# Kernel tuning notes

Hardware: AMD Instinct MI355X
Metric: run time of the kernel (lower is better)

The kernel has to match this reference:

```python
import jax, jax.numpy as jnp
import numpy as np

EMBED = 1024
HEADS = 16
HEAD_DIM = EMBED // HEADS


def setup_inputs() -> dict:
    key = jax.random.key(0)
    ks = jax.random.split(key, 8)
    B, S = 2, 2048
    inp = {
        "values": jax.random.normal(ks[0], (B, S, EMBED), jnp.float32),
        "keys": jax.random.normal(ks[1], (B, S, EMBED), jnp.float32),
        "queries": jax.random.normal(ks[2], (B, S, EMBED), jnp.float32),
        # per-head projection weights (torch Linear: y = x @ W.T), shared across heads
        "Wv": jax.random.normal(ks[3], (HEAD_DIM, HEAD_DIM), jnp.float32) / np.sqrt(HEAD_DIM),
        "Wk": jax.random.normal(ks[4], (HEAD_DIM, HEAD_DIM), jnp.float32) / np.sqrt(HEAD_DIM),
        "Wq": jax.random.normal(ks[5], (HEAD_DIM, HEAD_DIM), jnp.float32) / np.sqrt(HEAD_DIM),
        "Wo": jax.random.normal(ks[6], (EMBED, EMBED), jnp.float32) / np.sqrt(EMBED),
        "bo": jax.random.normal(ks[7], (EMBED,), jnp.float32) * 0.02,
    }
    return inp


def reference(values, keys, queries, Wv, Wk, Wq, Wo, bo):
    B, S, _ = queries.shape
    # split heads: (B, H, S, D)
    def split(x):
        return x.reshape(B, -1, HEADS, HEAD_DIM).transpose(0, 2, 1, 3)
    v, k, q = split(values), split(keys), split(queries)
    # per-head linear projections (no bias): x @ W.T
    v = jnp.einsum('bhsd,ed->bhse', v, Wv)
    k = jnp.einsum('bhsd,ed->bhse', k, Wk)
    q = jnp.einsum('bhsd,ed->bhse', q, Wq)
    # scaled dot-product attention (naive, full matrix)
    scores = jnp.einsum('bhqd,bhkd->bhqk', q, k) / jnp.sqrt(jnp.float32(HEAD_DIM))
    attn = jax.nn.softmax(scores, axis=-1)
    out = jnp.einsum('bhqk,bhkd->bhqd', attn, v)
    # merge heads and output projection
    out = out.transpose(0, 2, 1, 3).reshape(B, S, EMBED)
    return out @ Wo.T + bo
```

## Files before the change

kernel.cpp:

```cpp
#include <hip/hip_runtime.h>
#include <stdint.h>

#define HEADS 16
#define HD    64
#define SEQ   2048
#define BATCH 2
#define EMB   1024

using short8  = __attribute__((ext_vector_type(8))) short;
using float4v = __attribute__((ext_vector_type(4))) float;
using f32x16  = __attribute__((ext_vector_type(16))) float;

__device__ __forceinline__ unsigned int f2bfr(float f) {
    return (__float_as_uint(f) + 0x8000u) >> 16;
}

__device__ __forceinline__ unsigned int cvt_pk_bf16(float lo, float hi) {
    unsigned int r;
    asm("v_cvt_pk_bf16_f32 %0, %1, %2" : "=v"(r) : "v"(lo), "v"(hi));
    return r;
}

__device__ __forceinline__ short8 mk8(unsigned int a, unsigned int b,
                                      unsigned int c, unsigned int d) {
    union { unsigned int u[4]; short8 s; } x;
    x.u[0] = a; x.u[1] = b; x.u[2] = c; x.u[3] = d;
    return x.s;
}

__global__ __launch_bounds__(256) void cvt_wo_kernel(const float* __restrict__ Wo,
                                                     unsigned short* __restrict__ Wob) {
    int i = (blockIdx.x * 256 + threadIdx.x) * 4;
    float4 v = *(const float4*)(Wo + i);
    uint2 o;
    o.x = f2bfr(v.x) | (f2bfr(v.y) << 16);
    o.y = f2bfr(v.z) | (f2bfr(v.w) << 16);
    *(uint2*)(Wob + i) = o;
}

__global__ __launch_bounds__(256) void proj_kernel(
    const float* __restrict__ Vx, const float* __restrict__ Kx, const float* __restrict__ Qx,
    const float* __restrict__ Wv, const float* __restrict__ Wk, const float* __restrict__ Wq,
    unsigned short* __restrict__ Qp, unsigned short* __restrict__ Kp,
    unsigned short* __restrict__ Vt) {
    __shared__ __align__(16) unsigned short Ws[64 * 72];
    __shared__ __align__(16) unsigned short xs[64 * 72];
    __shared__ __align__(16) unsigned short vt2[64 * 72];

    const int t = threadIdx.x, w = t >> 6, lane = t & 63, cl = lane & 15, quad = lane >> 4;
    const int z  = blockIdx.z;
    const int bh = blockIdx.y;
    const int b  = bh >> 4, h = bh & 15;
    const int s0 = blockIdx.x * 64;

    const float* x = (z == 0) ? Qx : (z == 1) ? Kx : Vx;
    const float* W = (z == 0) ? Wq : (z == 1) ? Wk : Wv;
    const float scale = (z == 0) ? 0.18033688011112044f : 1.0f;

#pragma unroll
    for (int rep = 0; rep < 4; ++rep) {
        int idx = rep * 1024 + t * 4;
        int e = idx >> 6, d0 = idx & 63;
        float4 w4 = *(const float4*)(W + idx);
        uint2 pk;
        pk.x = f2bfr(w4.x * scale) | (f2bfr(w4.y * scale) << 16);
        pk.y = f2bfr(w4.z * scale) | (f2bfr(w4.w * scale) << 16);
        *(uint2*)(&Ws[e * 72 + d0]) = pk;

        int s = e;
        float4 v4 = *(const float4*)(x + (size_t)(b * SEQ + s0 + s) * EMB + h * 64 + d0);
        uint2 px;
        px.x = f2bfr(v4.x) | (f2bfr(v4.y) << 16);
        px.y = f2bfr(v4.z) | (f2bfr(v4.w) << 16);
        *(uint2*)(&xs[s * 72 + d0]) = px;
    }
    __syncthreads();

    short8 a0 = *(const short8*)(&xs[(w * 16 + cl) * 72 + quad * 8]);
    short8 a1 = *(const short8*)(&xs[(w * 16 + cl) * 72 + 32 + quad * 8]);
    float4v c[4];
#pragma unroll
    for (int nt = 0; nt < 4; ++nt) c[nt] = (float4v){0.f, 0.f, 0.f, 0.f};
#pragma unroll
    for (int nt = 0; nt < 4; ++nt) {
        short8 b0 = *(const short8*)(&Ws[(nt * 16 + cl) * 72 + quad * 8]);
        c[nt] = __builtin_amdgcn_mfma_f32_16x16x32_bf16(a0, b0, c[nt], 0, 0, 0);
        short8 b1 = *(const short8*)(&Ws[(nt * 16 + cl) * 72 + 32 + quad * 8]);
        c[nt] = __builtin_amdgcn_mfma_f32_16x16x32_bf16(a1, b1, c[nt], 0, 0, 0);
    }

    if (z < 2) {
#pragma unroll
        for (int nt = 0; nt < 4; ++nt)
#pragma unroll
            for (int r = 0; r < 4; ++r)
                xs[(w * 16 + quad * 4 + r) * 72 + nt * 16 + cl] =
                    (unsigned short)f2bfr(c[nt][r]);
        unsigned short* outp = (z == 0) ? Qp : Kp;
        int sl = w * 16 + (lane >> 2), c0 = (lane & 3) * 16;
        uint4 o0 = *(const uint4*)(&xs[sl * 72 + c0]);
        uint4 o1 = *(const uint4*)(&xs[sl * 72 + c0 + 8]);
        size_t base = ((size_t)bh * SEQ + s0 + sl) * 64 + c0;
        *(uint4*)(outp + base)     = o0;
        *(uint4*)(outp + base + 8) = o1;
    } else {
#pragma unroll
        for (int nt = 0; nt < 4; ++nt)
#pragma unroll
            for (int r = 0; r < 4; ++r)
                vt2[(nt * 16 + cl) * 72 + w * 16 + quad * 4 + r] =
                    (unsigned short)f2bfr(c[nt][r]);
        __syncthreads();
        int e = t >> 2, sc0 = (t & 3) * 16;
        uint4 o0 = *(const uint4*)(&vt2[e * 72 + sc0]);
        uint4 o1 = *(const uint4*)(&vt2[e * 72 + sc0 + 8]);
        size_t base = ((size_t)bh * 64 + e) * SEQ + s0 + sc0;
        *(uint4*)(Vt + base)     = o0;
        *(uint4*)(Vt + base + 8) = o1;
    }
}

__global__ __launch_bounds__(256) void attn_kernel(
    const unsigned short* __restrict__ Qp, const unsigned short* __restrict__ Kp,
    const unsigned short* __restrict__ Vt, unsigned short* __restrict__ AO) {
    __shared__ __align__(16) unsigned short Ks[2][64 * 72];
    __shared__ __align__(16) unsigned short Vs[2][64 * 72];

    const int t = threadIdx.x;
    const int w = t >> 6, lane = t & 63;
    const int l31 = lane & 31, h = lane >> 5;

    const int lid = blockIdx.x;
    const int bh  = ((lid & 7) << 2) | ((lid >> 3) & 3);
    const int q0  = (lid >> 5) * 128;

    const size_t hbase = (size_t)bh * SEQ * 64;
    const unsigned short* Kbase = Kp + hbase;
    const unsigned short* Vbase = Vt + hbase;

    short8 qf[4];
    {
        const unsigned short* qr = Qp + hbase + (size_t)(q0 + w * 32 + l31) * 64 + h * 8;
#pragma unroll
        for (int dt = 0; dt < 4; ++dt) qf[dt] = *(const short8*)(qr + dt * 16);
    }

    short8 ones;
#pragma unroll
    for (int i = 0; i < 8; ++i) ones[i] = (short)0x3F80;

    f32x16 o0, o1, ls;
#pragma unroll
    for (int r = 0; r < 16; ++r) { o0[r] = 0.f; o1[r] = 0.f; ls[r] = 0.f; }

    const int srow = t >> 3;
    const int scol = (t & 7) * 8;

    uint4 kreg[2], vreg[2];
#pragma unroll
    for (int p = 0; p < 2; ++p) {
        int row = srow + p * 32;
        kreg[p] = *(const uint4*)(Kbase + row * 64 + scol);
        vreg[p] = *(const uint4*)(Vbase + (size_t)row * SEQ + scol);
    }

    for (int kc = 0; kc < SEQ / 64; ++kc) {
        const int buf = kc & 1;
#pragma unroll
        for (int p = 0; p < 2; ++p) {
            int row = srow + p * 32;
            *(uint4*)(&Ks[buf][row * 72 + scol]) = kreg[p];
            *(uint4*)(&Vs[buf][row * 72 + scol]) = vreg[p];
        }
        __syncthreads();
        if (kc + 1 < SEQ / 64) {
#pragma unroll
            for (int p = 0; p < 2; ++p) {
                int row = srow + p * 32;
                kreg[p] = *(const uint4*)(Kbase + (size_t)(kc + 1) * 4096 + row * 64 + scol);
                vreg[p] = *(const uint4*)(Vbase + (size_t)row * SEQ + (kc + 1) * 64 + scol);
            }
        }

        f32x16 s0, s1;
#pragma unroll
        for (int r = 0; r < 16; ++r) { s0[r] = 0.f; s1[r] = 0.f; }

        __builtin_amdgcn_s_setprio(1);
#pragma unroll
        for (int dt = 0; dt < 4; ++dt) {
            short8 k0 = *(const short8*)(&Ks[buf][l31 * 72 + dt * 16 + h * 8]);
            short8 k1 = *(const short8*)(&Ks[buf][(32 + l31) * 72 + dt * 16 + h * 8]);
            s0 = __builtin_amdgcn_mfma_f32_32x32x16_bf16(k0, qf[dt], s0, 0, 0, 0);
            s1 = __builtin_amdgcn_mfma_f32_32x32x16_bf16(k1, qf[dt], s1, 0, 0, 0);
        }
        __builtin_amdgcn_s_setprio(0);

#pragma unroll
        for (int r = 0; r < 16; ++r) {
            s0[r] = __builtin_amdgcn_exp2f(s0[r]);
            s1[r] = __builtin_amdgcn_exp2f(s1[r]);
        }

        short8 fr[4];
        {
            unsigned e0 = cvt_pk_bf16(s0[0],  s0[1]),  e1 = cvt_pk_bf16(s0[2],  s0[3]);
            unsigned e2 = cvt_pk_bf16(s0[4],  s0[5]),  e3 = cvt_pk_bf16(s0[6],  s0[7]);
            unsigned e4 = cvt_pk_bf16(s0[8],  s0[9]),  e5 = cvt_pk_bf16(s0[10], s0[11]);
            unsigned e6 = cvt_pk_bf16(s0[12], s0[13]), e7 = cvt_pk_bf16(s0[14], s0[15]);
            unsigned x0 = __shfl_xor(e0, 32), x1 = __shfl_xor(e1, 32);
            unsigned x2 = __shfl_xor(e2, 32), x3 = __shfl_xor(e3, 32);
            unsigned x4 = __shfl_xor(e4, 32), x5 = __shfl_xor(e5, 32);
            unsigned x6 = __shfl_xor(e6, 32), x7 = __shfl_xor(e7, 32);
            fr[0] = mk8(h ? x2 : e0, h ? x3 : e1, h ? e2 : x0, h ? e3 : x1);
            fr[1] = mk8(h ? x6 : e4, h ? x7 : e5, h ? e6 : x4, h ? e7 : x5);
        }
        {
            unsigned e0 = cvt_pk_bf16(s1[0],  s1[1]),  e1 = cvt_pk_bf16(s1[2],  s1[3]);
            unsigned e2 = cvt_pk_bf16(s1[4],  s1[5]),  e3 = cvt_pk_bf16(s1[6],  s1[7]);
            unsigned e4 = cvt_pk_bf16(s1[8],  s1[9]),  e5 = cvt_pk_bf16(s1[10], s1[11]);
            unsigned e6 = cvt_pk_bf16(s1[12], s1[13]), e7 = cvt_pk_bf16(s1[14], s1[15]);
            unsigned x0 = __shfl_xor(e0, 32), x1 = __shfl_xor(e1, 32);
            unsigned x2 = __shfl_xor(e2, 32), x3 = __shfl_xor(e3, 32);
            unsigned x4 = __shfl_xor(e4, 32), x5 = __shfl_xor(e5, 32);
            unsigned x6 = __shfl_xor(e6, 32), x7 = __shfl_xor(e7, 32);
            fr[2] = mk8(h ? x2 : e0, h ? x3 : e1, h ? e2 : x0, h ? e3 : x1);
            fr[3] = mk8(h ? x6 : e4, h ? x7 : e5, h ? e6 : x4, h ? e7 : x5);
        }

        __builtin_amdgcn_s_setprio(1);
#pragma unroll
        for (int c = 0; c < 4; ++c) {
            short8 bv0 = *(const short8*)(&Vs[buf][l31 * 72 + c * 16 + h * 8]);
            short8 bv1 = *(const short8*)(&Vs[buf][(32 + l31) * 72 + c * 16 + h * 8]);
            o0 = __builtin_amdgcn_mfma_f32_32x32x16_bf16(fr[c], bv0, o0, 0, 0, 0);
            o1 = __builtin_amdgcn_mfma_f32_32x32x16_bf16(fr[c], bv1, o1, 0, 0, 0);
            ls = __builtin_amdgcn_mfma_f32_32x32x16_bf16(fr[c], ones, ls, 0, 0, 0);
        }
        __builtin_amdgcn_s_setprio(0);
    }

    float inv[16];
#pragma unroll
    for (int r = 0; r < 16; ++r) inv[r] = 1.0f / ls[r];
#pragma unroll
    for (int r = 0; r < 16; ++r) {
        int row = q0 + w * 32 + (r & 3) + 8 * (r >> 2) + 4 * h;
        size_t rb = hbase + (size_t)row * 64 + l31;
        AO[rb]      = (unsigned short)f2bfr(o0[r] * inv[r]);
        AO[rb + 32] = (unsigned short)f2bfr(o1[r] * inv[r]);
    }
}

__global__ __launch_bounds__(256) void outproj_kernel(
    const unsigned short* __restrict__ AO, const unsigned short* __restrict__ Wob,
    const float* __restrict__ bo, float* __restrict__ out) {
    __shared__ __align__(16) unsigned short As[2][64 * 72];
    __shared__ __align__(16) unsigned short Bs[2][64 * 72];

    const int t = threadIdx.x, w = t >> 6, lane = t & 63, cl = lane & 15, quad = lane >> 4;
    const int e0 = blockIdx.x * 64;
    const int m0 = blockIdx.y * 64;
    const int srow = t >> 3, scol = (t & 7) * 8;

    float4v c[4];
#pragma unroll
    for (int nt = 0; nt < 4; ++nt) c[nt] = (float4v){0.f, 0.f, 0.f, 0.f};

    uint4 areg[2], breg[2];
#pragma unroll
    for (int p = 0; p < 2; ++p) {
        int i = srow + p * 32;
        int r = m0 + i, b = r >> 11, s = r & 2047;
        areg[p] = *(const uint4*)(AO + ((size_t)(b * 16 + 0) * SEQ + s) * 64 + scol);
        breg[p] = *(const uint4*)(Wob + (size_t)(e0 + i) * EMB + scol);
    }

    for (int hc = 0; hc < 16; ++hc) {
        const int buf = hc & 1;
#pragma unroll
        for (int p = 0; p < 2; ++p) {
            int i = srow + p * 32;
            *(uint4*)(&As[buf][i * 72 + scol]) = areg[p];
            *(uint4*)(&Bs[buf][i * 72 + scol]) = breg[p];
        }
        __syncthreads();
        if (hc + 1 < 16) {
#pragma unroll
            for (int p = 0; p < 2; ++p) {
                int i = srow + p * 32;
                int r = m0 + i, b = r >> 11, s = r & 2047;
                areg[p] = *(const uint4*)(AO + ((size_t)(b * 16 + hc + 1) * SEQ + s) * 64 + scol);
                breg[p] = *(const uint4*)(Wob + (size_t)(e0 + i) * EMB + (hc + 1) * 64 + scol);
            }
        }
#pragma unroll
        for (int s2i = 0; s2i < 2; ++s2i) {
            short8 a = *(const short8*)(&As[buf][(w * 16 + cl) * 72 + s2i * 32 + quad * 8]);
#pragma unroll
            for (int nt = 0; nt < 4; ++nt) {
                short8 bb = *(const short8*)(&Bs[buf][(nt * 16 + cl) * 72 + s2i * 32 + quad * 8]);
                c[nt] = __builtin_amdgcn_mfma_f32_16x16x32_bf16(a, bb, c[nt], 0, 0, 0);
            }
        }
    }

#pragma unroll
    for (int nt = 0; nt < 4; ++nt) {
        float bias = bo[e0 + nt * 16 + cl];
#pragma unroll
        for (int r = 0; r < 4; ++r) {
            int row = m0 + w * 16 + quad * 4 + r;
            out[(size_t)row * EMB + e0 + nt * 16 + cl] = c[nt][r] + bias;
        }
    }
}

extern "C" void kernel_launch(void* const* d_in, const int* in_sizes, int n_in,
                              void* d_out, int out_size, void* d_ws, size_t ws_size,
                              hipStream_t stream) {
    const float* values  = (const float*)d_in[0];
    const float* keys    = (const float*)d_in[1];
    const float* queries = (const float*)d_in[2];
    const float* Wv = (const float*)d_in[3];
    const float* Wk = (const float*)d_in[4];
    const float* Wq = (const float*)d_in[5];
    const float* Wo = (const float*)d_in[6];
    const float* bo = (const float*)d_in[7];
    float* out = (float*)d_out;

    char* ws = (char*)d_ws;
    unsigned short* Qp  = (unsigned short*)(ws);
    unsigned short* Kp  = (unsigned short*)(ws + (8u  << 20));
    unsigned short* Vt  = (unsigned short*)(ws + (16u << 20));
    unsigned short* AO  = (unsigned short*)(ws + (24u << 20));
    unsigned short* Wob = (unsigned short*)(ws + (32u << 20));

    cvt_wo_kernel<<<dim3(1024), dim3(256), 0, stream>>>(Wo, Wob);
    proj_kernel<<<dim3(SEQ / 64, BATCH * HEADS, 3), dim3(256), 0, stream>>>(
        values, keys, queries, Wv, Wk, Wq, Qp, Kp, Vt);
    attn_kernel<<<dim3((SEQ / 128) * BATCH * HEADS), dim3(256), 0, stream>>>(Qp, Kp, Vt, AO);
    outproj_kernel<<<dim3(EMB / 64, (BATCH * SEQ) / 64), dim3(256), 0, stream>>>(
        AO, Wob, bo, out);
}
```

Baseline: 258.0 us.

## Rewrite output projection as LDS-free per-wave 32x64 MFMA tiles

```diff
diff --git a/kernel.cpp b/kernel.cpp
--- a/kernel.cpp
+++ b/kernel.cpp
@@ -235,7 +235,7 @@
             short8 bv1 = *(const short8*)(&Vs[buf][(32 + l31) * 72 + c * 16 + h * 8]);
             o0 = __builtin_amdgcn_mfma_f32_32x32x16_bf16(fr[c], bv0, o0, 0, 0, 0);
             o1 = __builtin_amdgcn_mfma_f32_32x32x16_bf16(fr[c], bv1, o1, 0, 0, 0);
-            ls = __builtin_amdgcn_mfma_f32_32x32x16_bf16(fr[c], ones, ls, 0, 0, 0);
+            ls = __builtin_amdgcn_mfma_f32_32x32x16_bf16(fr[c], ones,  ls, 0, 0, 0);
         }
         __builtin_amdgcn_s_setprio(0);
     }
@@ -255,64 +255,43 @@
 __global__ __launch_bounds__(256) void outproj_kernel(
     const unsigned short* __restrict__ AO, const unsigned short* __restrict__ Wob,
     const float* __restrict__ bo, float* __restrict__ out) {
-    __shared__ __align__(16) unsigned short As[2][64 * 72];
-    __shared__ __align__(16) unsigned short Bs[2][64 * 72];
-
-    const int t = threadIdx.x, w = t >> 6, lane = t & 63, cl = lane & 15, quad = lane >> 4;
-    const int e0 = blockIdx.x * 64;
-    const int m0 = blockIdx.y * 64;
-    const int srow = t >> 3, scol = (t & 7) * 8;
-
-    float4v c[4];
-#pragma unroll
-    for (int nt = 0; nt < 4; ++nt) c[nt] = (float4v){0.f, 0.f, 0.f, 0.f};
-
-    uint4 areg[2], breg[2];
-#pragma unroll
-    for (int p = 0; p < 2; ++p) {
-        int i = srow + p * 32;
-        int r = m0 + i, b = r >> 11, s = r & 2047;
-        areg[p] = *(const uint4*)(AO + ((size_t)(b * 16 + 0) * SEQ + s) * 64 + scol);
-        breg[p] = *(const uint4*)(Wob + (size_t)(e0 + i) * EMB + scol);
-    }
-
-    for (int hc = 0; hc < 16; ++hc) {
-        const int buf = hc & 1;
-#pragma unroll
-        for (int p = 0; p < 2; ++p) {
-            int i = srow + p * 32;
-            *(uint4*)(&As[buf][i * 72 + scol]) = areg[p];
-            *(uint4*)(&Bs[buf][i * 72 + scol]) = breg[p];
-        }
-        __syncthreads();
-        if (hc + 1 < 16) {
-#pragma unroll
-            for (int p = 0; p < 2; ++p) {
-                int i = srow + p * 32;
-                int r = m0 + i, b = r >> 11, s = r & 2047;
-                areg[p] = *(const uint4*)(AO + ((size_t)(b * 16 + hc + 1) * SEQ + s) * 64 + scol);
-                breg[p] = *(const uint4*)(Wob + (size_t)(e0 + i) * EMB + (hc + 1) * 64 + scol);
-            }
-        }
-#pragma unroll
-        for (int s2i = 0; s2i < 2; ++s2i) {
-            short8 a = *(const short8*)(&As[buf][(w * 16 + cl) * 72 + s2i * 32 + quad * 8]);
-#pragma unroll
-            for (int nt = 0; nt < 4; ++nt) {
-                short8 bb = *(const short8*)(&Bs[buf][(nt * 16 + cl) * 72 + s2i * 32 + quad * 8]);
-                c[nt] = __builtin_amdgcn_mfma_f32_16x16x32_bf16(a, bb, c[nt], 0, 0, 0);
-            }
-        }
-    }
-
-#pragma unroll
-    for (int nt = 0; nt < 4; ++nt) {
-        float bias = bo[e0 + nt * 16 + cl];
-#pragma unroll
-        for (int r = 0; r < 4; ++r) {
-            int row = m0 + w * 16 + quad * 4 + r;
-            out[(size_t)row * EMB + e0 + nt * 16 + cl] = c[nt][r] + bias;
-        }
+    const int t = threadIdx.x, w = t >> 6, lane = t & 63;
+    const int l31 = lane & 31, h = lane >> 5;
+
+    const int wid = blockIdx.x * 4 + w;
+    const int mt  = wid >> 4;
+    const int et  = wid & 15;
+    const int m0  = mt * 32, e0 = et * 64;
+    const int b   = m0 >> 11;
+    const int s   = (m0 & 2047) + l31;
+
+    const unsigned short* pA  = AO + ((size_t)(b * 16) * SEQ + s) * 64 + h * 8;
+    const unsigned short* pB0 = Wob + (size_t)(e0 + l31) * EMB + h * 8;
+    const unsigned short* pB1 = Wob + (size_t)(e0 + 32 + l31) * EMB + h * 8;
+
+    f32x16 c0, c1;
+#pragma unroll
+    for (int r = 0; r < 16; ++r) { c0[r] = 0.f; c1[r] = 0.f; }
+
+    for (int hh = 0; hh < 16; ++hh) {
+#pragma unroll
+        for (int k4 = 0; k4 < 4; ++k4) {
+            short8 a  = *(const short8*)(pA + k4 * 16);
+            short8 b0 = *(const short8*)(pB0 + hh * 64 + k4 * 16);
+            short8 b1 = *(const short8*)(pB1 + hh * 64 + k4 * 16);
+            c0 = __builtin_amdgcn_mfma_f32_32x32x16_bf16(a, b0, c0, 0, 0, 0);
+            c1 = __builtin_amdgcn_mfma_f32_32x32x16_bf16(a, b1, c1, 0, 0, 0);
+        }
+        pA += (size_t)SEQ * 64;
+    }
+
+    const float bias0 = bo[e0 + l31];
+    const float bias1 = bo[e0 + 32 + l31];
+#pragma unroll
+    for (int r = 0; r < 16; ++r) {
+        int m = m0 + (r & 3) + 8 * (r >> 2) + 4 * h;
+        out[(size_t)m * EMB + e0 + l31]      = c0[r] + bias0;
+        out[(size_t)m * EMB + e0 + 32 + l31] = c1[r] + bias1;
     }
 }
 
@@ -340,6 +319,6 @@
     proj_kernel<<<dim3(SEQ / 64, BATCH * HEADS, 3), dim3(256), 0, stream>>>(
         values, keys, queries, Wv, Wk, Wq, Qp, Kp, Vt);
     attn_kernel<<<dim3((SEQ / 128) * BATCH * HEADS), dim3(256), 0, stream>>>(Qp, Kp, Vt, AO);
-    outproj_kernel<<<dim3(EMB / 64, (BATCH * SEQ) / 64), dim3(256), 0, stream>>>(
+    outproj_kernel<<<dim3((EMB / 64) * ((BATCH * SEQ) / 32) / 4), dim3(256), 0, stream>>>(
         AO, Wob, bo, out);
 }
```

After: 231.3 us. 10.4% less time.
